# Kernel tuning notes

Measured on AMD Instinct MI355X. Metric: run time of the kernel, lower is better.

The kernel has to match this reference:

```python
import jax, jax.numpy as jnp
import numpy as np

DIM = 256
HEADS = 8
HEAD_DIM = DIM // HEADS
EPS = 1e-5


def layer_norm(x, g, b):
    mu = jnp.mean(x, axis=-1, keepdims=True)
    var = jnp.mean(jnp.square(x - mu), axis=-1, keepdims=True)
    return (x - mu) * jax.lax.rsqrt(var + EPS) * g + b


def setup_inputs() -> dict:
    key = jax.random.key(0)
    ks = jax.random.split(key, 10)
    s = 0.02
    return {
        "x": jax.random.normal(ks[0], (4, DIM, 64, 64), dtype=jnp.float32),
        "g1": jnp.ones((DIM,), jnp.float32),
        "b1": jnp.zeros((DIM,), jnp.float32),
        "Wqkv": jax.random.normal(ks[1], (DIM, 3 * DIM), jnp.float32) * s,
        "Wp": jax.random.normal(ks[2], (DIM, DIM), jnp.float32) * s,
        "bp": jnp.zeros((DIM,), jnp.float32),
        "g2": jnp.ones((DIM,), jnp.float32),
        "b2": jnp.zeros((DIM,), jnp.float32),
        "W1": jax.random.normal(ks[3], (DIM, 2 * DIM), jnp.float32) * s,
        "bf1": jnp.zeros((2 * DIM,), jnp.float32),
        "W2": jax.random.normal(ks[4], (2 * DIM, DIM), jnp.float32) * s,
        "bf2": jnp.zeros((DIM,), jnp.float32),
    }


def reference(x, g1, b1, Wqkv, Wp, bp, g2, b2, W1, bf1, W2, bf2):
    B, C, H, W = x.shape
    N = H * W
    scale = HEAD_DIM ** -0.5
    tokens = x.reshape(B, C, N).transpose(0, 2, 1)  # [B,N,C]
    t = layer_norm(tokens, g1, b1)
    qkv = (t @ Wqkv).reshape(B, N, 3, HEADS, HEAD_DIM)
    q = qkv[:, :, 0].transpose(0, 2, 1, 3)  # [B,h,N,d]
    k = qkv[:, :, 1].transpose(0, 2, 1, 3)
    v = qkv[:, :, 2].transpose(0, 2, 1, 3)
    attn = jax.nn.softmax(jnp.einsum("bhnd,bhmd->bhnm", q, k) * scale, axis=-1)
    out = jnp.einsum("bhnm,bhmd->bhnd", attn, v)
    out = out.transpose(0, 2, 1, 3).reshape(B, N, C)
    tokens = tokens + out @ Wp + bp
    t2 = layer_norm(tokens, g2, b2)
    h = jax.nn.gelu(t2 @ W1 + bf1, approximate=False)
    tokens = tokens + h @ W2 + bf2
    return tokens.transpose(0, 2, 1).reshape(B, C, H, W)
```

## Files before the change

kernel.cpp:

```cpp
#include <hip/hip_runtime.h>

typedef unsigned short u16;
typedef unsigned int   u32;

using bf16x8 = __attribute__((ext_vector_type(8))) __bf16;
using f32x4  = __attribute__((ext_vector_type(4))) float;
using f32x16 = __attribute__((ext_vector_type(16))) float;

#define MFMA16(a, b, c) __builtin_amdgcn_mfma_f32_16x16x32_bf16((a), (b), (c), 0, 0, 0)
#define MFMA32(a, b, c) __builtin_amdgcn_mfma_f32_32x32x16_bf16((a), (b), (c), 0, 0, 0)

__device__ inline u16 f2bf(float f) {
  u32 x = __float_as_uint(f);
  return (u16)((x + 0x7FFFu + ((x >> 16) & 1u)) >> 16);
}

__device__ inline const bf16x8* bfp(const u16* p) {
  return reinterpret_cast<const bf16x8*>(p);
}

__global__ __launch_bounds__(256) void k_pre(
    const float* __restrict__ x, const float* __restrict__ g1,
    const float* __restrict__ b1, float* __restrict__ tokens,
    u16* __restrict__ ln,
    const float* __restrict__ Wqkv, const float* __restrict__ Wp,
    const float* __restrict__ W1,   const float* __restrict__ W2,
    u16* __restrict__ wqkvT, u16* __restrict__ wpT,
    u16* __restrict__ w1T,   u16* __restrict__ w2T) {
  __shared__ float tile[256][33];
  __shared__ float red[2][8][32];
  __shared__ float stat[2][32];
  int tid = threadIdx.x;
  if (blockIdx.x >= 512) {
    int blk = blockIdx.x - 512;
    const float* src; u16* dst; int R, C, t;
    if (blk < 192)      { src = Wqkv; dst = wqkvT; R = 256; C = 768; t = blk; }
    else if (blk < 256) { src = Wp;   dst = wpT;   R = 256; C = 256; t = blk - 192; }
    else if (blk < 384) { src = W1;   dst = w1T;   R = 256; C = 512; t = blk - 256; }
    else                { src = W2;   dst = w2T;   R = 512; C = 256; t = blk - 384; }
    int tpc = C >> 5;
    int tr = (t / tpc) << 5, tc = (t % tpc) << 5;
    int j = tid & 31, iq = tid >> 5;
    #pragma unroll
    for (int i = 0; i < 4; ++i)
      tile[iq + 8 * i][j] = src[(size_t)(tr + iq + 8 * i) * C + tc + j];
    __syncthreads();
    #pragma unroll
    for (int i = 0; i < 4; ++i)
      dst[(size_t)(tc + iq + 8 * i) * R + tr + j] = f2bf(tile[j][iq + 8 * i]);
    return;
  }
  int blk = blockIdx.x;
  int b = blk >> 7, n0 = (blk & 127) << 5;
  {
    int cq = tid >> 5, j = tid & 31;
    const float* xp = x + (((size_t)b * 256) << 12) + n0 + j;
    #pragma unroll 8
    for (int it = 0; it < 32; ++it) {
      int c = it * 8 + cq;
      tile[c][j] = xp[(size_t)c << 12];
    }
  }
  __syncthreads();
  {
    int tn = tid & 31, qq = tid >> 5;
    float s = 0.f, s2 = 0.f;
    #pragma unroll 8
    for (int i = 0; i < 32; ++i) {
      float v = tile[qq * 32 + i][tn];
      s += v; s2 += v * v;
    }
    red[0][qq][tn] = s; red[1][qq][tn] = s2;
  }
  __syncthreads();
  if (tid < 32) {
    float su = 0.f, sq = 0.f;
    #pragma unroll
    for (int qq = 0; qq < 8; ++qq) { su += red[0][qq][tid]; sq += red[1][qq][tid]; }
    float mu  = su * (1.f / 256.f);
    float var = sq * (1.f / 256.f) - mu * mu;
    stat[0][tid] = mu;
    stat[1][tid] = rsqrtf(var + 1e-5f);
  }
  __syncthreads();
  float g = g1[tid], bb = b1[tid];
  size_t base = ((size_t)(b * 4096 + n0)) * 256 + tid;
  for (int it = 0; it < 32; ++it) {
    float v = tile[tid][it];
    float y = (v - stat[0][it]) * stat[1][it] * g + bb;
    tokens[base + (size_t)it * 256] = v;
    ln[base + (size_t)it * 256] = f2bf(y);
  }
}

template <int K>
__device__ inline void mm16(const u16* __restrict__ A, const u16* __restrict__ BT,
                            int arow, int bcol, f32x4 acc[4]) {
  int lane = threadIdx.x & 63;
  int r = lane & 15, g = lane >> 4;
  const u16* ap  = A  + (size_t)(arow + r) * K + g * 8;
  const u16* bp0 = BT + (size_t)(bcol + r) * K + g * 8;
  #pragma unroll 4
  for (int k0 = 0; k0 < K; k0 += 32) {
    bf16x8 a = *bfp(ap + k0);
    #pragma unroll
    for (int nt = 0; nt < 4; ++nt) {
      bf16x8 b = *bfp(bp0 + nt * 16 * K + k0);
      acc[nt] = MFMA16(a, b, acc[nt]);
    }
  }
}

template <int K>
__device__ inline void mm32(const u16* __restrict__ A, const u16* __restrict__ BT,
                            int arow, int bcol, f32x4 acc[2][4]) {
  int lane = threadIdx.x & 63;
  int r = lane & 15, g = lane >> 4;
  const u16* ap0 = A  + (size_t)(arow + r) * K + g * 8;
  const u16* bp0 = BT + (size_t)(bcol + r) * K + g * 8;
  #pragma unroll 4
  for (int k0 = 0; k0 < K; k0 += 32) {
    bf16x8 a0 = *bfp(ap0 + k0);
    bf16x8 a1 = *bfp(ap0 + 16 * K + k0);
    #pragma unroll
    for (int nt = 0; nt < 4; ++nt) {
      bf16x8 b = *bfp(bp0 + nt * 16 * K + k0);
      acc[0][nt] = MFMA16(a0, b, acc[0][nt]);
      acc[1][nt] = MFMA16(a1, b, acc[1][nt]);
    }
  }
}

__global__ __launch_bounds__(256) void k_qkv(
    const u16* __restrict__ ln, const u16* __restrict__ wT,
    u16* __restrict__ q, u16* __restrict__ kf, u16* __restrict__ vf) {
  int w = threadIdx.x >> 6, lane = threadIdx.x & 63;
  int r16 = lane & 15, g4 = lane >> 4;
  int m0 = blockIdx.y * 128 + w * 32;
  int n0 = blockIdx.x * 64;
  f32x4 z = {0.f, 0.f, 0.f, 0.f};
  f32x4 acc[2][4] = {{z, z, z, z}, {z, z, z, z}};
  mm32<256>(ln, wT, m0, n0, acc);
  int b = m0 >> 12;
  const float qs = (float)(0.17677669529663687 * 1.4426950408889634);
  #pragma unroll
  for (int rg = 0; rg < 2; ++rg) {
    int nbase = (m0 & 4095) + rg * 16 + g4 * 4;
    #pragma unroll
    for (int nt = 0; nt < 4; ++nt) {
      int col = n0 + nt * 16 + r16;
      int which = col >> 8, h = (col >> 5) & 7, d = col & 31;
      size_t bh_off = ((size_t)(b * 8 + h)) << 17;
      if (which == 0) {
        #pragma unroll
        for (int r = 0; r < 4; ++r)
          q[((size_t)(b * 8 + h) * 4096 + nbase + r) * 32 + d] =
              f2bf(acc[rg][nt][r] * qs);
      } else if (which == 1) {
        int sel = d >> 4, lh = (d >> 3) & 1, jj = d & 7;
        #pragma unroll
        for (int r = 0; r < 4; ++r) {
          int key = nbase + r;
          kf[bh_off + (size_t)(key >> 5) * 1024 + sel * 512 +
             (((key & 31) | (lh << 5)) << 3) + jj] = f2bf(acc[rg][nt][r]);
        }
      } else {
        int kk = nbase & 31;
        int sel = kk >> 4, lh = (kk >> 3) & 1, j0 = kk & 7;
        ushort4 o4;
        o4.x = f2bf(acc[rg][nt][0]); o4.y = f2bf(acc[rg][nt][1]);
        o4.z = f2bf(acc[rg][nt][2]); o4.w = f2bf(acc[rg][nt][3]);
        *(ushort4*)(vf + bh_off + (size_t)(nbase >> 5) * 1024 + sel * 512 +
                    ((d | (lh << 5)) << 3) + j0) = o4;
      }
    }
  }
}

__global__ __launch_bounds__(512, 4) void k_attn(
    const u16* __restrict__ q, const u16* __restrict__ kf,
    const u16* __restrict__ vf, u16* __restrict__ attnout) {
  __shared__ float obuf[2][3][64][17];
  __shared__ float lsbuf[2][3][64];
  int lane = threadIdx.x & 63;
  int w = threadIdx.x >> 6;
  int qi = w >> 2, kj = w & 3;
  int r32 = lane & 31, hi = lane >> 5;
  int d = blockIdx.x;
  int bh = (d & 7) + 8 * (d >> 8);
  int qt = (d >> 3) & 31;
  int q0 = qt * 128 + qi * 64;
  const u16* qh = q + ((size_t)bh << 17);
  bf16x8 qf00 = *bfp(qh + (size_t)(q0 + r32) * 32 + hi * 8);
  bf16x8 qf01 = *bfp(qh + (size_t)(q0 + r32) * 32 + 16 + hi * 8);
  bf16x8 qf10 = *bfp(qh + (size_t)(q0 + 32 + r32) * 32 + hi * 8);
  bf16x8 qf11 = *bfp(qh + (size_t)(q0 + 32 + r32) * 32 + 16 + hi * 8);

  const u16* kp = kf + ((size_t)bh << 17) + (size_t)kj * 32768 + lane * 8;
  const u16* vp = vf + ((size_t)bh << 17) + (size_t)kj * 32768 + lane * 8;

  f32x16 o0, o1, zz;
  #pragma unroll
  for (int r = 0; r < 16; ++r) { o0[r] = 0.f; o1[r] = 0.f; zz[r] = 0.f; }
  float ls0 = 0.f, ls1 = 0.f;

  #pragma unroll 2
  for (int c = 0; c < 32; ++c) {
    bf16x8 ka0 = *bfp(kp);
    bf16x8 ka1 = *bfp(kp + 512);
    bf16x8 va0 = *bfp(vp);
    bf16x8 va1 = *bfp(vp + 512);
    kp += 1024; vp += 1024;

    {
      f32x16 s = MFMA32(ka0, qf00, zz);
      s = MFMA32(ka1, qf01, s);
      #pragma unroll
      for (int r = 0; r < 16; ++r) s[r] = __builtin_amdgcn_exp2f(s[r]);
      float t0 = ((s[0] + s[1]) + (s[2] + s[3])) + ((s[4] + s[5]) + (s[6] + s[7]));
      float t1 = ((s[8] + s[9]) + (s[10] + s[11])) + ((s[12] + s[13]) + (s[14] + s[15]));
      ls0 += t0 + t1;
      u32 c8[8];
      #pragma unroll
      for (int i = 0; i < 8; ++i)
        asm("v_cvt_pk_bf16_f32 %0, %1, %2" : "=v"(c8[i]) : "v"(s[2 * i]), "v"(s[2 * i + 1]));
      asm("v_permlane32_swap_b32 %0, %1" : "+v"(c8[0]), "+v"(c8[2]));
      asm("v_permlane32_swap_b32 %0, %1" : "+v"(c8[1]), "+v"(c8[3]));
      asm("v_permlane32_swap_b32 %0, %1" : "+v"(c8[4]), "+v"(c8[6]));
      asm("v_permlane32_swap_b32 %0, %1" : "+v"(c8[5]), "+v"(c8[7]));
      union { u32 u[4]; bf16x8 v; } pf0, pf1;
      pf0.u[0] = c8[0]; pf0.u[1] = c8[1]; pf0.u[2] = c8[2]; pf0.u[3] = c8[3];
      pf1.u[0] = c8[4]; pf1.u[1] = c8[5]; pf1.u[2] = c8[6]; pf1.u[3] = c8[7];
      o0 = MFMA32(va0, pf0.v, o0);
      o0 = MFMA32(va1, pf1.v, o0);
    }
    {
      f32x16 s = MFMA32(ka0, qf10, zz);
      s = MFMA32(ka1, qf11, s);
      #pragma unroll
      for (int r = 0; r < 16; ++r) s[r] = __builtin_amdgcn_exp2f(s[r]);
      float t0 = ((s[0] + s[1]) + (s[2] + s[3])) + ((s[4] + s[5]) + (s[6] + s[7]));
      float t1 = ((s[8] + s[9]) + (s[10] + s[11])) + ((s[12] + s[13]) + (s[14] + s[15]));
      ls1 += t0 + t1;
      u32 c8[8];
      #pragma unroll
      for (int i = 0; i < 8; ++i)
        asm("v_cvt_pk_bf16_f32 %0, %1, %2" : "=v"(c8[i]) : "v"(s[2 * i]), "v"(s[2 * i + 1]));
      asm("v_permlane32_swap_b32 %0, %1" : "+v"(c8[0]), "+v"(c8[2]));
      asm("v_permlane32_swap_b32 %0, %1" : "+v"(c8[1]), "+v"(c8[3]));
      asm("v_permlane32_swap_b32 %0, %1" : "+v"(c8[4]), "+v"(c8[6]));
      asm("v_permlane32_swap_b32 %0, %1" : "+v"(c8[5]), "+v"(c8[7]));
      union { u32 u[4]; bf16x8 v; } pf0, pf1;
      pf0.u[0] = c8[0]; pf0.u[1] = c8[1]; pf0.u[2] = c8[2]; pf0.u[3] = c8[3];
      pf1.u[0] = c8[4]; pf1.u[1] = c8[5]; pf1.u[2] = c8[6]; pf1.u[3] = c8[7];
      o1 = MFMA32(va0, pf0.v, o1);
      o1 = MFMA32(va1, pf1.v, o1);
    }
  }

  ls0 += __shfl_xor(ls0, 32);
  ls1 += __shfl_xor(ls1, 32);

  if (kj != 0) {
    #pragma unroll
    for (int g = 0; g < 16; ++g) obuf[qi][kj - 1][lane][g] = o0[g];
    lsbuf[qi][kj - 1][lane] = ls0;
  }
  __syncthreads();
  float inv0 = 0.f;
  if (kj == 0) {
    float lst = ls0 + lsbuf[qi][0][lane] + lsbuf[qi][1][lane] + lsbuf[qi][2][lane];
    inv0 = __builtin_amdgcn_rcpf(lst);
    #pragma unroll
    for (int g = 0; g < 16; ++g)
      o0[g] += obuf[qi][0][lane][g] + obuf[qi][1][lane][g] + obuf[qi][2][lane][g];
  }
  __syncthreads();
  if (kj != 0) {
    #pragma unroll
    for (int g = 0; g < 16; ++g) obuf[qi][kj - 1][lane][g] = o1[g];
    lsbuf[qi][kj - 1][lane] = ls1;
  }
  __syncthreads();
  if (kj == 0) {
    int b = bh >> 3, h = bh & 7;
    float lst1 = ls1 + lsbuf[qi][0][lane] + lsbuf[qi][1][lane] + lsbuf[qi][2][lane];
    float inv1 = __builtin_amdgcn_rcpf(lst1);
    #pragma unroll
    for (int g = 0; g < 16; ++g)
      o1[g] += obuf[qi][0][lane][g] + obuf[qi][1][lane][g] + obuf[qi][2][lane][g];
    size_t nrow0 = ((size_t)(b * 4096 + q0 + r32)) * 256 + h * 32;
    size_t nrow1 = ((size_t)(b * 4096 + q0 + 32 + r32)) * 256 + h * 32;
    #pragma unroll
    for (int g = 0; g < 4; ++g) {
      ushort4 ov;
      ov.x = f2bf(o0[g * 4 + 0] * inv0);
      ov.y = f2bf(o0[g * 4 + 1] * inv0);
      ov.z = f2bf(o0[g * 4 + 2] * inv0);
      ov.w = f2bf(o0[g * 4 + 3] * inv0);
      *(ushort4*)(attnout + nrow0 + g * 8 + hi * 4) = ov;
      ushort4 ow;
      ow.x = f2bf(o1[g * 4 + 0] * inv1);
      ow.y = f2bf(o1[g * 4 + 1] * inv1);
      ow.z = f2bf(o1[g * 4 + 2] * inv1);
      ow.w = f2bf(o1[g * 4 + 3] * inv1);
      *(ushort4*)(attnout + nrow1 + g * 8 + hi * 4) = ow;
    }
  }
}

__global__ __launch_bounds__(512) void k_post(
    const u16* __restrict__ ao, const u16* __restrict__ wpT,
    const float* __restrict__ bp, const float* __restrict__ g2,
    const float* __restrict__ b2, const float* __restrict__ tokens,
    const u16* __restrict__ w1T, const float* __restrict__ bf1,
    const u16* __restrict__ w2T, const float* __restrict__ bf2,
    float* __restrict__ out) {
  __shared__ u16 lnS[32][264];
  __shared__ u16 hS[32][520];
  __shared__ float red[2][2][4][16];
  int w = threadIdx.x >> 6, lane = threadIdx.x & 63;
  int r16 = lane & 15, g4 = lane >> 4;
  int rh = w & 1, cg = w >> 1;
  int m0 = blockIdx.x * 32;
  int row0 = m0 + rh * 16;

  f32x4 z = {0.f, 0.f, 0.f, 0.f};
  f32x4 tA[4] = {z, z, z, z};
  mm16<256>(ao, wpT, row0, cg * 64, tA);
  float sum[4] = {0.f, 0.f, 0.f, 0.f}, sq[4] = {0.f, 0.f, 0.f, 0.f};
  #pragma unroll
  for (int nt = 0; nt < 4; ++nt) {
    int col = cg * 64 + nt * 16 + r16;
    float bias = bp[col];
    #pragma unroll
    for (int r = 0; r < 4; ++r) {
      float v = tokens[(size_t)(row0 + g4 * 4 + r) * 256 + col] + tA[nt][r] + bias;
      tA[nt][r] = v;
      sum[r] += v; sq[r] += v * v;
    }
  }
  #pragma unroll
  for (int mask = 1; mask < 16; mask <<= 1) {
    #pragma unroll
    for (int r = 0; r < 4; ++r) {
      sum[r] += __shfl_xor(sum[r], mask);
      sq[r]  += __shfl_xor(sq[r], mask);
    }
  }
  if (r16 == 0) {
    #pragma unroll
    for (int r = 0; r < 4; ++r) {
      red[0][rh][cg][g4 * 4 + r] = sum[r];
      red[1][rh][cg][g4 * 4 + r] = sq[r];
    }
  }
  __syncthreads();
  {
    float mu[4], rs[4];
    #pragma unroll
    for (int r = 0; r < 4; ++r) {
      int ri = g4 * 4 + r;
      float S  = red[0][rh][0][ri] + red[0][rh][1][ri] + red[0][rh][2][ri] + red[0][rh][3][ri];
      float SQ = red[1][rh][0][ri] + red[1][rh][1][ri] + red[1][rh][2][ri] + red[1][rh][3][ri];
      mu[r] = S * (1.f / 256.f);
      rs[r] = rsqrtf(SQ * (1.f / 256.f) - mu[r] * mu[r] + 1e-5f);
    }
    #pragma unroll
    for (int nt = 0; nt < 4; ++nt) {
      int col = cg * 64 + nt * 16 + r16;
      float gg = g2[col], bb = b2[col];
      #pragma unroll
      for (int r = 0; r < 4; ++r)
        lnS[rh * 16 + g4 * 4 + r][col] = f2bf((tA[nt][r] - mu[r]) * rs[r] * gg + bb);
    }
  }
  __syncthreads();

  {
    f32x4 accB[8] = {z, z, z, z, z, z, z, z};
    const u16* apB = &lnS[rh * 16 + r16][g4 * 8];
    const u16* bpB = w1T + (size_t)(cg * 128 + r16) * 256 + g4 * 8;
    #pragma unroll 2
    for (int k0 = 0; k0 < 256; k0 += 32) {
      bf16x8 a = *bfp(apB + k0);
      #pragma unroll
      for (int nt = 0; nt < 8; ++nt) {
        bf16x8 b = *bfp(bpB + nt * 16 * 256 + k0);
        accB[nt] = MFMA16(a, b, accB[nt]);
      }
    }
    int rl = rh * 16 + g4 * 4;
    #pragma unroll
    for (int nt = 0; nt < 8; ++nt) {
      int col = cg * 128 + nt * 16 + r16;
      float bias = bf1[col];
      #pragma unroll
      for (int r = 0; r < 4; ++r) {
        float xx = accB[nt][r] + bias;
        float x2 = xx * xx;
        float zt = xx * (2.3021188f + 0.10293855f * x2);
        float e  = __builtin_amdgcn_exp2f(zt);
        float ge = xx * (1.f - __builtin_amdgcn_rcpf(1.f + e));
        hS[rl + r][col] = f2bf(ge);
      }
    }
  }
  __syncthreads();

  {
    f32x4 accC[4] = {z, z, z, z};
    const u16* apC = &hS[rh * 16 + r16][g4 * 8];
    const u16* bpC = w2T + (size_t)(cg * 64 + r16) * 512 + g4 * 8;
    #pragma unroll 4
    for (int k0 = 0; k0 < 512; k0 += 32) {
      bf16x8 a = *bfp(apC + k0);
      #pragma unroll
      for (int nt = 0; nt < 4; ++nt) {
        bf16x8 b = *bfp(bpC + nt * 16 * 512 + k0);
        accC[nt] = MFMA16(a, b, accC[nt]);
      }
    }
    int b = m0 >> 12;
    int nl = (m0 & 4095) + rh * 16 + g4 * 4;
    #pragma unroll
    for (int nt = 0; nt < 4; ++nt) {
      int col = cg * 64 + nt * 16 + r16;
      float bias = bf2[col];
      float4 o;
      o.x = tA[nt][0] + accC[nt][0] + bias;
      o.y = tA[nt][1] + accC[nt][1] + bias;
      o.z = tA[nt][2] + accC[nt][2] + bias;
      o.w = tA[nt][3] + accC[nt][3] + bias;
      *(float4*)(out + (((size_t)(b * 256 + col)) << 12) + nl) = o;
    }
  }
}

extern "C" void kernel_launch(void* const* d_in, const int* in_sizes, int n_in,
                              void* d_out, int out_size, void* d_ws, size_t ws_size,
                              hipStream_t stream) {
  (void)in_sizes; (void)n_in; (void)out_size; (void)ws_size;
  const float* x    = (const float*)d_in[0];
  const float* g1   = (const float*)d_in[1];
  const float* b1   = (const float*)d_in[2];
  const float* Wqkv = (const float*)d_in[3];
  const float* Wp   = (const float*)d_in[4];
  const float* bp   = (const float*)d_in[5];
  const float* g2   = (const float*)d_in[6];
  const float* b2   = (const float*)d_in[7];
  const float* W1   = (const float*)d_in[8];
  const float* bf1  = (const float*)d_in[9];
  const float* W2   = (const float*)d_in[10];
  const float* bf2  = (const float*)d_in[11];
  float* out = (float*)d_out;

  char* ws = (char*)d_ws;
  float* tokens = (float*)(ws);
  u16* lnb      = (u16*)(ws + 16777216);
  u16* qb       = (u16*)(ws + 25165824);
  u16* kfb      = (u16*)(ws + 33554432);
  u16* vfb      = (u16*)(ws + 41943040);
  u16* aob      = (u16*)(ws + 50331648);
  u16* wqkvT    = (u16*)(ws + 67108864);
  u16* wpT      = (u16*)(ws + 67502080);
  u16* w1T      = (u16*)(ws + 67633152);
  u16* w2T      = (u16*)(ws + 67895296);

  k_pre  <<<1024, 256, 0, stream>>>(x, g1, b1, tokens, lnb,
                                    Wqkv, Wp, W1, W2, wqkvT, wpT, w1T, w2T);
  k_qkv  <<<dim3(12, 128), 256, 0, stream>>>(lnb, wqkvT, qb, kfb, vfb);
  k_attn <<<1024, 512, 0, stream>>>(qb, kfb, vfb, aob);
  k_post <<<512, 512, 0, stream>>>(aob, wpT, bp, g2, b2, tokens,
                                   w1T, bf1, w2T, bf2, out);
}
```

Before: 216.8 us.

## Stage Q/K epilogue through LDS for vectorized stores; halve post-kernel row tile

The QKV kernel now writes its Q and K outputs into a transposed shared-memory tile, then emits 16-byte vectorized stores in the attention layouts instead of scattered 2-byte writes. V keeps its existing direct path. Separately, the post-attention MLP kernel processes 16 rows per block instead of 32, with each of 8 waves owning a column slice, which doubles the grid to 1024 blocks for better occupancy. The trade-off is extra LDS traffic and a barrier in the QKV epilogue, plus twice as many weight reads per output row in the post kernel.

```diff
diff --git a/kernel.cpp b/kernel.cpp
--- a/kernel.cpp
+++ b/kernel.cpp
@@ -4,6 +4,7 @@
 typedef unsigned int   u32;
 
 using bf16x8 = __attribute__((ext_vector_type(8))) __bf16;
+using u16x8  = __attribute__((ext_vector_type(8))) unsigned short;
 using f32x4  = __attribute__((ext_vector_type(4))) float;
 using f32x16 = __attribute__((ext_vector_type(16))) float;
 
@@ -134,37 +135,28 @@
 __global__ __launch_bounds__(256) void k_qkv(
     const u16* __restrict__ ln, const u16* __restrict__ wT,
     u16* __restrict__ q, u16* __restrict__ kf, u16* __restrict__ vf) {
-  int w = threadIdx.x >> 6, lane = threadIdx.x & 63;
+  __shared__ u16 tileT[64][136];
+  int tid = threadIdx.x;
+  int w = tid >> 6, lane = tid & 63;
   int r16 = lane & 15, g4 = lane >> 4;
   int m0 = blockIdx.y * 128 + w * 32;
-  int n0 = blockIdx.x * 64;
+  int bx = blockIdx.x;
+  int n0 = bx * 64;
   f32x4 z = {0.f, 0.f, 0.f, 0.f};
   f32x4 acc[2][4] = {{z, z, z, z}, {z, z, z, z}};
   mm32<256>(ln, wT, m0, n0, acc);
-  int b = m0 >> 12;
-  const float qs = (float)(0.17677669529663687 * 1.4426950408889634);
-  #pragma unroll
-  for (int rg = 0; rg < 2; ++rg) {
-    int nbase = (m0 & 4095) + rg * 16 + g4 * 4;
-    #pragma unroll
-    for (int nt = 0; nt < 4; ++nt) {
-      int col = n0 + nt * 16 + r16;
-      int which = col >> 8, h = (col >> 5) & 7, d = col & 31;
-      size_t bh_off = ((size_t)(b * 8 + h)) << 17;
-      if (which == 0) {
-        #pragma unroll
-        for (int r = 0; r < 4; ++r)
-          q[((size_t)(b * 8 + h) * 4096 + nbase + r) * 32 + d] =
-              f2bf(acc[rg][nt][r] * qs);
-      } else if (which == 1) {
-        int sel = d >> 4, lh = (d >> 3) & 1, jj = d & 7;
-        #pragma unroll
-        for (int r = 0; r < 4; ++r) {
-          int key = nbase + r;
-          kf[bh_off + (size_t)(key >> 5) * 1024 + sel * 512 +
-             (((key & 31) | (lh << 5)) << 3) + jj] = f2bf(acc[rg][nt][r]);
-        }
-      } else {
+  int b = blockIdx.y >> 5;
+  const float qsc = (float)(0.17677669529663687 * 1.4426950408889634);
+
+  if (bx >= 8) {
+    #pragma unroll
+    for (int rg = 0; rg < 2; ++rg) {
+      int nbase = (m0 & 4095) + rg * 16 + g4 * 4;
+      #pragma unroll
+      for (int nt = 0; nt < 4; ++nt) {
+        int col = n0 + nt * 16 + r16;
+        int h = (col >> 5) & 7, d = col & 31;
+        size_t bh_off = ((size_t)(b * 8 + h)) << 17;
         int kk = nbase & 31;
         int sel = kk >> 4, lh = (kk >> 3) & 1, j0 = kk & 7;
         ushort4 o4;
@@ -173,6 +165,51 @@
         *(ushort4*)(vf + bh_off + (size_t)(nbase >> 5) * 1024 + sel * 512 +
                     ((d | (lh << 5)) << 3) + j0) = o4;
       }
+    }
+    return;
+  }
+
+  float sc = (bx < 4) ? qsc : 1.0f;
+  #pragma unroll
+  for (int rg = 0; rg < 2; ++rg) {
+    #pragma unroll
+    for (int nt = 0; nt < 4; ++nt) {
+      ushort4 t4;
+      t4.x = f2bf(acc[rg][nt][0] * sc);
+      t4.y = f2bf(acc[rg][nt][1] * sc);
+      t4.z = f2bf(acc[rg][nt][2] * sc);
+      t4.w = f2bf(acc[rg][nt][3] * sc);
+      *(ushort4*)&tileT[nt * 16 + r16][w * 32 + rg * 16 + g4 * 4] = t4;
+    }
+  }
+  __syncthreads();
+
+  if (bx < 4) {
+    int hl = tid >> 7, nl = tid & 127;
+    size_t bh_off = ((size_t)(b * 8 + bx * 2 + hl)) << 17;
+    int nwb = (blockIdx.y & 31) * 128 + nl;
+    u16* dst = q + bh_off + (size_t)nwb * 32;
+    #pragma unroll
+    for (int i = 0; i < 4; ++i) {
+      int d0 = i * 8;
+      union { u16 s[8]; u16x8 v; } pk;
+      #pragma unroll
+      for (int j = 0; j < 8; ++j) pk.s[j] = tileT[hl * 32 + d0 + j][nl];
+      *(u16x8*)(dst + d0) = pk.v;
+    }
+  } else {
+    int l = tid & 63;
+    #pragma unroll
+    for (int i = 0; i < 4; ++i) {
+      int u = (tid >> 6) + i * 4;
+      int hl = u >> 3, chunk = (u >> 1) & 3, sel = u & 1;
+      size_t bh_off = ((size_t)(b * 8 + (bx - 4) * 2 + hl)) << 17;
+      int gchunk = (blockIdx.y & 31) * 4 + chunk;
+      union { u16 s[8]; u16x8 v; } pk;
+      #pragma unroll
+      for (int j = 0; j < 8; ++j)
+        pk.s[j] = tileT[hl * 32 + sel * 16 + (l >> 5) * 8 + j][chunk * 32 + (l & 31)];
+      *(u16x8*)(kf + bh_off + (size_t)gchunk * 1024 + sel * 512 + l * 8) = pk.v;
     }
   }
 }
@@ -316,26 +353,35 @@
     const u16* __restrict__ w1T, const float* __restrict__ bf1,
     const u16* __restrict__ w2T, const float* __restrict__ bf2,
     float* __restrict__ out) {
-  __shared__ u16 lnS[32][264];
-  __shared__ u16 hS[32][520];
-  __shared__ float red[2][2][4][16];
+  __shared__ u16 lnS[16][264];
+  __shared__ u16 hS[16][520];
+  __shared__ float red[2][8][16];
   int w = threadIdx.x >> 6, lane = threadIdx.x & 63;
   int r16 = lane & 15, g4 = lane >> 4;
-  int rh = w & 1, cg = w >> 1;
-  int m0 = blockIdx.x * 32;
-  int row0 = m0 + rh * 16;
-
+  int m0 = blockIdx.x * 16;
   f32x4 z = {0.f, 0.f, 0.f, 0.f};
-  f32x4 tA[4] = {z, z, z, z};
-  mm16<256>(ao, wpT, row0, cg * 64, tA);
+
+  f32x4 tA[2] = {z, z};
+  {
+    const u16* ap = ao  + (size_t)(m0 + r16) * 256 + g4 * 8;
+    const u16* bp0 = wpT + (size_t)(w * 32 + r16) * 256 + g4 * 8;
+    #pragma unroll 4
+    for (int k0 = 0; k0 < 256; k0 += 32) {
+      bf16x8 a = *bfp(ap + k0);
+      bf16x8 b0 = *bfp(bp0 + k0);
+      bf16x8 b1 = *bfp(bp0 + 16 * 256 + k0);
+      tA[0] = MFMA16(a, b0, tA[0]);
+      tA[1] = MFMA16(a, b1, tA[1]);
+    }
+  }
   float sum[4] = {0.f, 0.f, 0.f, 0.f}, sq[4] = {0.f, 0.f, 0.f, 0.f};
   #pragma unroll
-  for (int nt = 0; nt < 4; ++nt) {
-    int col = cg * 64 + nt * 16 + r16;
+  for (int nt = 0; nt < 2; ++nt) {
+    int col = w * 32 + nt * 16 + r16;
     float bias = bp[col];
     #pragma unroll
     for (int r = 0; r < 4; ++r) {
-      float v = tokens[(size_t)(row0 + g4 * 4 + r) * 256 + col] + tA[nt][r] + bias;
+      float v = tokens[(size_t)(m0 + g4 * 4 + r) * 256 + col] + tA[nt][r] + bias;
       tA[nt][r] = v;
       sum[r] += v; sq[r] += v * v;
     }
@@ -351,8 +397,8 @@
   if (r16 == 0) {
     #pragma unroll
     for (int r = 0; r < 4; ++r) {
-      red[0][rh][cg][g4 * 4 + r] = sum[r];
-      red[1][rh][cg][g4 * 4 + r] = sq[r];
+      red[0][w][g4 * 4 + r] = sum[r];
+      red[1][w][g4 * 4 + r] = sq[r];
     }
   }
   __syncthreads();
@@ -361,39 +407,39 @@
     #pragma unroll
     for (int r = 0; r < 4; ++r) {
       int ri = g4 * 4 + r;
-      float S  = red[0][rh][0][ri] + red[0][rh][1][ri] + red[0][rh][2][ri] + red[0][rh][3][ri];
-      float SQ = red[1][rh][0][ri] + red[1][rh][1][ri] + red[1][rh][2][ri] + red[1][rh][3][ri];
+      float S = 0.f, SQ = 0.f;
+      #pragma unroll
+      for (int w2 = 0; w2 < 8; ++w2) { S += red[0][w2][ri]; SQ += red[1][w2][ri]; }
       mu[r] = S * (1.f / 256.f);
       rs[r] = rsqrtf(SQ * (1.f / 256.f) - mu[r] * mu[r] + 1e-5f);
     }
     #pragma unroll
-    for (int nt = 0; nt < 4; ++nt) {
-      int col = cg * 64 + nt * 16 + r16;
+    for (int nt = 0; nt < 2; ++nt) {
+      int col = w * 32 + nt * 16 + r16;
       float gg = g2[col], bb = b2[col];
       #pragma unroll
       for (int r = 0; r < 4; ++r)
-        lnS[rh * 16 + g4 * 4 + r][col] = f2bf((tA[nt][r] - mu[r]) * rs[r] * gg + bb);
+        lnS[g4 * 4 + r][col] = f2bf((tA[nt][r] - mu[r]) * rs[r] * gg + bb);
     }
   }
   __syncthreads();
 
   {
-    f32x4 accB[8] = {z, z, z, z, z, z, z, z};
-    const u16* apB = &lnS[rh * 16 + r16][g4 * 8];
-    const u16* bpB = w1T + (size_t)(cg * 128 + r16) * 256 + g4 * 8;
-    #pragma unroll 2
+    f32x4 accB[4] = {z, z, z, z};
+    const u16* apB = &lnS[r16][g4 * 8];
+    const u16* bpB = w1T + (size_t)(w * 64 + r16) * 256 + g4 * 8;
+    #pragma unroll 4
     for (int k0 = 0; k0 < 256; k0 += 32) {
       bf16x8 a = *bfp(apB + k0);
       #pragma unroll
-      for (int nt = 0; nt < 8; ++nt) {
+      for (int nt = 0; nt < 4; ++nt) {
         bf16x8 b = *bfp(bpB + nt * 16 * 256 + k0);
         accB[nt] = MFMA16(a, b, accB[nt]);
       }
     }
-    int rl = rh * 16 + g4 * 4;
-    #pragma unroll
-    for (int nt = 0; nt < 8; ++nt) {
-      int col = cg * 128 + nt * 16 + r16;
+    #pragma unroll
+    for (int nt = 0; nt < 4; ++nt) {
+      int col = w * 64 + nt * 16 + r16;
       float bias = bf1[col];
       #pragma unroll
       for (int r = 0; r < 4; ++r) {
@@ -402,30 +448,29 @@
         float zt = xx * (2.3021188f + 0.10293855f * x2);
         float e  = __builtin_amdgcn_exp2f(zt);
         float ge = xx * (1.f - __builtin_amdgcn_rcpf(1.f + e));
-        hS[rl + r][col] = f2bf(ge);
+        hS[g4 * 4 + r][col] = f2bf(ge);
       }
     }
   }
   __syncthreads();
 
   {
-    f32x4 accC[4] = {z, z, z, z};
-    const u16* apC = &hS[rh * 16 + r16][g4 * 8];
-    const u16* bpC = w2T + (size_t)(cg * 64 + r16) * 512 + g4 * 8;
+    f32x4 accC[2] = {z, z};
+    const u16* apC = &hS[r16][g4 * 8];
+    const u16* bpC = w2T + (size_t)(w * 32 + r16) * 512 + g4 * 8;
     #pragma unroll 4
     for (int k0 = 0; k0 < 512; k0 += 32) {
       bf16x8 a = *bfp(apC + k0);
-      #pragma unroll
-      for (int nt = 0; nt < 4; ++nt) {
-        bf16x8 b = *bfp(bpC + nt * 16 * 512 + k0);
-        accC[nt] = MFMA16(a, b, accC[nt]);
-      }
+      bf16x8 b0 = *bfp(bpC + k0);
+      bf16x8 b1 = *bfp(bpC + 16 * 512 + k0);
+      accC[0] = MFMA16(a, b0, accC[0]);
+      accC[1] = MFMA16(a, b1, accC[1]);
     }
     int b = m0 >> 12;
-    int nl = (m0 & 4095) + rh * 16 + g4 * 4;
-    #pragma unroll
-    for (int nt = 0; nt < 4; ++nt) {
-      int col = cg * 64 + nt * 16 + r16;
+    int nl = (m0 & 4095) + g4 * 4;
+    #pragma unroll
+    for (int nt = 0; nt < 2; ++nt) {
+      int col = w * 32 + nt * 16 + r16;
       float bias = bf2[col];
       float4 o;
       o.x = tA[nt][0] + accC[nt][0] + bias;
@@ -471,6 +516,6 @@
                                     Wqkv, Wp, W1, W2, wqkvT, wpT, w1T, w2T);
   k_qkv  <<<dim3(12, 128), 256, 0, stream>>>(lnb, wqkvT, qb, kfb, vfb);
   k_attn <<<1024, 512, 0, stream>>>(qb, kfb, vfb, aob);
-  k_post <<<512, 512, 0, stream>>>(aob, wpT, bp, g2, b2, tokens,
-                                   w1T, bf1, w2T, bf2, out);
-}
+  k_post <<<1024, 512, 0, stream>>>(aob, wpT, bp, g2, b2, tokens,
+                                    w1T, bf1, w2T, bf2, out);
+}
```

After: 223.0 us. 2.9% more time.
